# Performance work log

Hardware: AMD Instinct MI355X
Metric: run time of the kernel (lower is better)

## Reference

```python
import jax, jax.numpy as jnp
import numpy as np
from jax import lax

B, W, L, K = 256, 4096, 16, 8  # batch, nodes/level, levels, fan-in


def setup_inputs() -> dict:
    key = jax.random.key(0)
    ks = jax.random.split(key, 7)
    s = 1.0 / np.sqrt(K)  # torch nn.Linear default init scale
    observed_bits = jnp.round(jax.random.uniform(ks[0], (B, W))).astype(jnp.float32)
    prior_w = jax.random.uniform(ks[1], (W,), minval=-1.0, maxval=1.0)  # PriorNode Linear(1,1) weight
    prior_b = jax.random.uniform(ks[2], (W,), minval=-1.0, maxval=1.0)
    weights = jax.random.uniform(ks[3], (L - 1, W, K), minval=-s, maxval=s)  # per-node Linear(K,1)
    biases = jax.random.uniform(ks[4], (L - 1, W), minval=-s, maxval=s)
    # parents sorted DESCENDING per node: heap pops higher rv first, so inputs are
    # concatenated in descending parent-rv order in the original traversal.
    parents = -jnp.sort(-jax.random.randint(ks[5], (L - 1, W, K), 0, W), axis=-1)
    inv_mask = jax.random.randint(ks[6], (L - 1, W), 0, 2).astype(bool)  # True -> InvNode
    return {"observed_bits": observed_bits, "prior_w": prior_w, "prior_b": prior_b,
            "weights": weights, "biases": biases, "parents": parents, "inv_mask": inv_mask}


def reference(observed_bits, prior_w, prior_b, weights, biases, parents, inv_mask):
    # Observed level: PriorNode with num_parents=1 -> relu(w*bit + b), per node.  (B, W)
    h = jax.nn.relu(observed_bits * prior_w[None, :] + prior_b[None, :])

    def step(h, lvl):
        w, b, p, inv = lvl  # (W,K), (W,), (W,K) int, (W,) bool
        x = h[:, p]                                   # gather parent outputs -> (B, W, K)
        x = jnp.where(inv[:, None], 1.0 - x, x)       # InvNode applies fc(1 - x)
        h2 = jax.nn.relu(jnp.einsum('bnk,nk->bn', x, w) + b)  # per-node Linear(K,1)+ReLU
        return h2, None

    h, _ = lax.scan(step, h, (weights, biases, parents, inv_mask))
    return h  # (B, num_input_bits) == pred.squeeze() of the original
```

## Files before the change

### kernel.cpp

```cpp
#include <hip/hip_runtime.h>

#define WN 4096
#define BN 256
#define KN 8
#define NLVL 15
#define BSPLIT 2
#define NBLK (BN / BSPLIT)
#define NTHR 1024
#define NPT (WN / NTHR)

__global__ __launch_bounds__(NTHR) void fused_lds_kernel(
    const float* __restrict__ obs, const float* __restrict__ pw,
    const float* __restrict__ pb,  const float* __restrict__ wts,
    const float* __restrict__ bia, const int* __restrict__ par,
    const int* __restrict__ inv,   float* __restrict__ out) {
  __shared__ float h[2][BSPLIT][WN];
  const int t  = threadIdx.x;
  const int b0 = blockIdx.x * BSPLIT;

#pragma unroll
  for (int i = 0; i < NPT; ++i) {
    const int n  = i * NTHR + t;
    const float w = pw[n], bb = pb[n];
#pragma unroll
    for (int c = 0; c < BSPLIT; ++c)
      h[0][c][n] = fmaxf(fmaf(obs[(size_t)(b0 + c) * WN + n], w, bb), 0.0f);
  }
  __syncthreads();

  int cur = 0;
  for (int l = 0; l < NLVL; ++l) {
    const float* wl = wts + (size_t)l * WN * KN;
    const int*   pl = par + (size_t)l * WN * KN;
    const float* bl = bia + (size_t)l * WN;
    const int*   il = inv + (size_t)l * WN;
    const float* hc0 = h[cur][0];
    const float* hc1 = h[cur][1];
    float*       hn0 = h[cur ^ 1][0];
    float*       hn1 = h[cur ^ 1][1];
#pragma unroll
    for (int i = 0; i < NPT; ++i) {
      const int n = i * NTHR + t;
      const int4   p0 = *(const int4*)(pl + (size_t)n * KN);
      const int4   p1 = *(const int4*)(pl + (size_t)n * KN + 4);
      float4       w0 = *(const float4*)(wl + (size_t)n * KN);
      float4       w1 = *(const float4*)(wl + (size_t)n * KN + 4);
      const float  bb = bl[n];
      const bool   iv = il[n] != 0;
      const float ws  = ((w0.x + w0.y) + (w0.z + w0.w)) + ((w1.x + w1.y) + (w1.z + w1.w));
      const float base = iv ? bb + ws : bb;
      const float s    = iv ? -1.0f : 1.0f;
      w0.x *= s; w0.y *= s; w0.z *= s; w0.w *= s;
      w1.x *= s; w1.y *= s; w1.z *= s; w1.w *= s;

      float a0 = base, a1 = base;
      a0 = fmaf(hc0[p0.x], w0.x, a0);  a1 = fmaf(hc1[p0.x], w0.x, a1);
      a0 = fmaf(hc0[p0.y], w0.y, a0);  a1 = fmaf(hc1[p0.y], w0.y, a1);
      a0 = fmaf(hc0[p0.z], w0.z, a0);  a1 = fmaf(hc1[p0.z], w0.z, a1);
      a0 = fmaf(hc0[p0.w], w0.w, a0);  a1 = fmaf(hc1[p0.w], w0.w, a1);
      a0 = fmaf(hc0[p1.x], w1.x, a0);  a1 = fmaf(hc1[p1.x], w1.x, a1);
      a0 = fmaf(hc0[p1.y], w1.y, a0);  a1 = fmaf(hc1[p1.y], w1.y, a1);
      a0 = fmaf(hc0[p1.z], w1.z, a0);  a1 = fmaf(hc1[p1.z], w1.z, a1);
      a0 = fmaf(hc0[p1.w], w1.w, a0);  a1 = fmaf(hc1[p1.w], w1.w, a1);

      hn0[n] = fmaxf(a0, 0.0f);
      hn1[n] = fmaxf(a1, 0.0f);
    }
    __syncthreads();
    cur ^= 1;
  }

#pragma unroll
  for (int i = 0; i < NPT; ++i) {
    const int n = i * NTHR + t;
#pragma unroll
    for (int c = 0; c < BSPLIT; ++c)
      out[(size_t)(b0 + c) * WN + n] = h[cur][c][n];
  }
}

extern "C" void kernel_launch(void* const* d_in, const int* in_sizes, int n_in,
                              void* d_out, int out_size, void* d_ws, size_t ws_size,
                              hipStream_t stream) {
  const float* obs = (const float*)d_in[0];
  const float* pw  = (const float*)d_in[1];
  const float* pb  = (const float*)d_in[2];
  const float* wts = (const float*)d_in[3];
  const float* bia = (const float*)d_in[4];
  const int*   par = (const int*)d_in[5];
  const int*   inv = (const int*)d_in[6];
  float* out = (float*)d_out;

  fused_lds_kernel<<<NBLK, NTHR, 0, stream>>>(obs, pw, pb, wts, bia, par, inv, out);
}
```

Measured before the change: 129.6 us.

## Precompute signed weights and packed 16-bit parents in a prep kernel, one batch per block

A new prep kernel folds the InvNode sign flip and bias adjustment into the weights and packs the parent indices as 16-bit pairs. It writes these to workspace, and the main kernel reads the preprocessed data instead of recomputing it per block. The main kernel also drops from two batch rows per block to one, launching 256 blocks with half the LDS each. This cuts per-block parameter bandwidth and ALU work, but adds a second kernel launch and halves the reuse of each parameter load across batch rows.

Result: faster. 116.4 us (-10.2%).

```diff
diff --git a/kernel.cpp b/kernel.cpp
--- a/kernel.cpp
+++ b/kernel.cpp
@@ -4,67 +4,70 @@
 #define BN 256
 #define KN 8
 #define NLVL 15
-#define BSPLIT 2
-#define NBLK (BN / BSPLIT)
 #define NTHR 1024
 #define NPT (WN / NTHR)
 
+__global__ __launch_bounds__(256) void prep_kernel(
+    const float* __restrict__ wts, const float* __restrict__ bia,
+    const int* __restrict__ par,   const int* __restrict__ inv,
+    float4* __restrict__ Wp, uint4* __restrict__ Pp, float* __restrict__ Bz) {
+  const int idx = blockIdx.x * 256 + threadIdx.x;
+  const float4 w0 = *(const float4*)(wts + (size_t)idx * KN);
+  const float4 w1 = *(const float4*)(wts + (size_t)idx * KN + 4);
+  const int4   p0 = *(const int4*)(par + (size_t)idx * KN);
+  const int4   p1 = *(const int4*)(par + (size_t)idx * KN + 4);
+  const bool   iv = inv[idx] != 0;
+  const float  ws = ((w0.x + w0.y) + (w0.z + w0.w)) + ((w1.x + w1.y) + (w1.z + w1.w));
+  const float  s  = iv ? -1.0f : 1.0f;
+  Wp[(size_t)idx * 2]     = make_float4(w0.x * s, w0.y * s, w0.z * s, w0.w * s);
+  Wp[(size_t)idx * 2 + 1] = make_float4(w1.x * s, w1.y * s, w1.z * s, w1.w * s);
+  uint4 pp;
+  pp.x = (unsigned)p0.x | ((unsigned)p0.y << 16);
+  pp.y = (unsigned)p0.z | ((unsigned)p0.w << 16);
+  pp.z = (unsigned)p1.x | ((unsigned)p1.y << 16);
+  pp.w = (unsigned)p1.z | ((unsigned)p1.w << 16);
+  Pp[idx] = pp;
+  Bz[idx] = iv ? bia[idx] + ws : bia[idx];
+}
+
 __global__ __launch_bounds__(NTHR) void fused_lds_kernel(
     const float* __restrict__ obs, const float* __restrict__ pw,
-    const float* __restrict__ pb,  const float* __restrict__ wts,
-    const float* __restrict__ bia, const int* __restrict__ par,
-    const int* __restrict__ inv,   float* __restrict__ out) {
-  __shared__ float h[2][BSPLIT][WN];
-  const int t  = threadIdx.x;
-  const int b0 = blockIdx.x * BSPLIT;
+    const float* __restrict__ pb,  const float4* __restrict__ Wp,
+    const uint4* __restrict__ Pp,  const float* __restrict__ Bz,
+    float* __restrict__ out) {
+  __shared__ float h[2][WN];
+  const int    t = threadIdx.x;
+  const size_t b = blockIdx.x;
 
 #pragma unroll
   for (int i = 0; i < NPT; ++i) {
-    const int n  = i * NTHR + t;
-    const float w = pw[n], bb = pb[n];
-#pragma unroll
-    for (int c = 0; c < BSPLIT; ++c)
-      h[0][c][n] = fmaxf(fmaf(obs[(size_t)(b0 + c) * WN + n], w, bb), 0.0f);
+    const int n = i * NTHR + t;
+    h[0][n] = fmaxf(fmaf(obs[b * WN + n], pw[n], pb[n]), 0.0f);
   }
   __syncthreads();
 
   int cur = 0;
   for (int l = 0; l < NLVL; ++l) {
-    const float* wl = wts + (size_t)l * WN * KN;
-    const int*   pl = par + (size_t)l * WN * KN;
-    const float* bl = bia + (size_t)l * WN;
-    const int*   il = inv + (size_t)l * WN;
-    const float* hc0 = h[cur][0];
-    const float* hc1 = h[cur][1];
-    float*       hn0 = h[cur ^ 1][0];
-    float*       hn1 = h[cur ^ 1][1];
+    const float* hc = h[cur];
+    float*       hn = h[cur ^ 1];
+    const size_t lb = (size_t)l * WN;
 #pragma unroll
     for (int i = 0; i < NPT; ++i) {
-      const int n = i * NTHR + t;
-      const int4   p0 = *(const int4*)(pl + (size_t)n * KN);
-      const int4   p1 = *(const int4*)(pl + (size_t)n * KN + 4);
-      float4       w0 = *(const float4*)(wl + (size_t)n * KN);
-      float4       w1 = *(const float4*)(wl + (size_t)n * KN + 4);
-      const float  bb = bl[n];
-      const bool   iv = il[n] != 0;
-      const float ws  = ((w0.x + w0.y) + (w0.z + w0.w)) + ((w1.x + w1.y) + (w1.z + w1.w));
-      const float base = iv ? bb + ws : bb;
-      const float s    = iv ? -1.0f : 1.0f;
-      w0.x *= s; w0.y *= s; w0.z *= s; w0.w *= s;
-      w1.x *= s; w1.y *= s; w1.z *= s; w1.w *= s;
-
-      float a0 = base, a1 = base;
-      a0 = fmaf(hc0[p0.x], w0.x, a0);  a1 = fmaf(hc1[p0.x], w0.x, a1);
-      a0 = fmaf(hc0[p0.y], w0.y, a0);  a1 = fmaf(hc1[p0.y], w0.y, a1);
-      a0 = fmaf(hc0[p0.z], w0.z, a0);  a1 = fmaf(hc1[p0.z], w0.z, a1);
-      a0 = fmaf(hc0[p0.w], w0.w, a0);  a1 = fmaf(hc1[p0.w], w0.w, a1);
-      a0 = fmaf(hc0[p1.x], w1.x, a0);  a1 = fmaf(hc1[p1.x], w1.x, a1);
-      a0 = fmaf(hc0[p1.y], w1.y, a0);  a1 = fmaf(hc1[p1.y], w1.y, a1);
-      a0 = fmaf(hc0[p1.z], w1.z, a0);  a1 = fmaf(hc1[p1.z], w1.z, a1);
-      a0 = fmaf(hc0[p1.w], w1.w, a0);  a1 = fmaf(hc1[p1.w], w1.w, a1);
-
-      hn0[n] = fmaxf(a0, 0.0f);
-      hn1[n] = fmaxf(a1, 0.0f);
+      const int    n  = i * NTHR + t;
+      const size_t nl = lb + n;
+      const uint4  pp = Pp[nl];
+      const float4 w0 = Wp[nl * 2];
+      const float4 w1 = Wp[nl * 2 + 1];
+      float acc = Bz[nl];
+      acc = fmaf(hc[pp.x & 0xffffu], w0.x, acc);
+      acc = fmaf(hc[pp.x >> 16],     w0.y, acc);
+      acc = fmaf(hc[pp.y & 0xffffu], w0.z, acc);
+      acc = fmaf(hc[pp.y >> 16],     w0.w, acc);
+      acc = fmaf(hc[pp.z & 0xffffu], w1.x, acc);
+      acc = fmaf(hc[pp.z >> 16],     w1.y, acc);
+      acc = fmaf(hc[pp.w & 0xffffu], w1.z, acc);
+      acc = fmaf(hc[pp.w >> 16],     w1.w, acc);
+      hn[n] = fmaxf(acc, 0.0f);
     }
     __syncthreads();
     cur ^= 1;
@@ -73,9 +76,7 @@
 #pragma unroll
   for (int i = 0; i < NPT; ++i) {
     const int n = i * NTHR + t;
-#pragma unroll
-    for (int c = 0; c < BSPLIT; ++c)
-      out[(size_t)(b0 + c) * WN + n] = h[cur][c][n];
+    out[b * WN + n] = h[cur][n];
   }
 }
 
@@ -91,5 +92,11 @@
   const int*   inv = (const int*)d_in[6];
   float* out = (float*)d_out;
 
-  fused_lds_kernel<<<NBLK, NTHR, 0, stream>>>(obs, pw, pb, wts, bia, par, inv, out);
+  char* ws = (char*)d_ws;
+  float4* Wp = (float4*)ws;
+  uint4*  Pp = (uint4*)(ws + (size_t)NLVL * WN * 32);
+  float*  Bz = (float*)(ws + (size_t)NLVL * WN * 48);
+
+  prep_kernel<<<(NLVL * WN) / 256, 256, 0, stream>>>(wts, bia, par, inv, Wp, Pp, Bz);
+  fused_lds_kernel<<<BN, NTHR, 0, stream>>>(obs, pw, pb, Wp, Pp, Bz, out);
 }
```
